# Kernel optimization log

Measured on AMD Instinct MI355X. Metric: run time of the kernel, lower is better.

## Reference

```python
import jax, jax.numpy as jnp
import numpy as np

N = 20000
E = 320000
D = 256
OUT = 256
NEG_SLOPE = 0.2


def setup_inputs() -> dict:
    key = jax.random.key(0)
    ks = jax.random.split(key, 16)
    s = 1.0 / np.sqrt(D)
    x = jax.random.normal(ks[0], (N, D), dtype=jnp.float32)
    edge_index = jax.random.randint(ks[1], (2, E), 0, N, dtype=jnp.int64)
    W1 = jax.random.uniform(ks[2], (D, D), jnp.float32, -s, s)
    W2 = jax.random.uniform(ks[3], (D, D), jnp.float32, -s, s)
    Ws = jax.random.uniform(ks[4], (6, D, D), jnp.float32, -s, s)      # per-layer GATConv lin weight
    a_src = jax.random.uniform(ks[5], (6, D), jnp.float32, -s, s)      # per-layer att_src
    a_dst = jax.random.uniform(ks[6], (6, D), jnp.float32, -s, s)      # per-layer att_dst
    bias = jnp.zeros((6, D), dtype=jnp.float32)                        # per-layer GATConv bias
    W3 = jax.random.uniform(ks[7], (2 * D, OUT), jnp.float32, -s, s)
    return {"x": x, "edge_index": edge_index, "W1": W1, "W2": W2,
            "Ws": Ws, "a_src": a_src, "a_dst": a_dst, "bias": bias, "W3": W3}


def _gat_layer(h, src, dst, W, asrc, adst, b):
    # h: [N, D] -> linear transform
    hw = h @ W                                         # [N, D]
    e_src = hw @ asrc                                  # [N]
    e_dst = hw @ adst                                  # [N]
    e = jax.nn.leaky_relu(e_src[src] + e_dst[dst], NEG_SLOPE)  # [E]
    # softmax over incoming edges per destination node
    m = jax.ops.segment_max(e, dst, num_segments=N)    # [N], -inf for empty segs (unused)
    ee = jnp.exp(e - m[dst])                           # [E]
    denom = jax.ops.segment_sum(ee, dst, num_segments=N)
    alpha = ee / denom[dst]                            # [E]
    msg = alpha[:, None] * hw[src]                     # [E, D]
    out = jax.ops.segment_sum(msg, dst, num_segments=N)  # [N, D]
    return out + b


def reference(x, edge_index, W1, W2, Ws, a_src, a_dst, bias, W3):
    src, dst = edge_index[0], edge_index[1]
    h = x @ W1
    h = h @ W2
    for i in range(6):
        h = _gat_layer(h, src, dst, Ws[i], a_src[i], a_dst[i], bias[i])
    h = jnp.concatenate((h, h), axis=1)   # [N, 2D]
    h = jax.nn.relu(h)
    return h @ W3                          # [N, OUT]
```

## Files before the change

### kernel.cpp

```cpp
#include <hip/hip_runtime.h>
#include <hip/hip_fp16.h>
#include <stdint.h>

#define NNODES 20000
#define EEDGES 320000
#define DD     256
#define NEG_SLOPE 0.2f
#define SCAN_BLOCKS ((NNODES + 255) / 256)

typedef _Float16 half8 __attribute__((ext_vector_type(8)));
typedef _Float16 half4 __attribute__((ext_vector_type(4)));
typedef float f32x4 __attribute__((ext_vector_type(4)));


__global__ void zero_ints_k(int* __restrict__ p, int n) {
    int i = blockIdx.x * 256 + threadIdx.x;
    if (i < n) p[i] = 0;
}

__global__ void hist_k(const int* __restrict__ dst, int* __restrict__ rowptr) {
    int i = blockIdx.x * 256 + threadIdx.x;
    if (i < EEDGES) atomicAdd(&rowptr[dst[i] + 1], 1);
}

__global__ __launch_bounds__(256) void scan1_k(int* __restrict__ rowptr, int* __restrict__ bsums) {
    __shared__ int buf[256];
    int idx = blockIdx.x * 256 + threadIdx.x;
    int v = (idx < NNODES) ? rowptr[idx + 1] : 0;
    buf[threadIdx.x] = v;
    __syncthreads();
#pragma unroll
    for (int off = 1; off < 256; off <<= 1) {
        int t = (threadIdx.x >= (unsigned)off) ? buf[threadIdx.x - off] : 0;
        __syncthreads();
        buf[threadIdx.x] += t;
        __syncthreads();
    }
    if (idx < NNODES) rowptr[idx + 1] = buf[threadIdx.x];
    if (threadIdx.x == 255) bsums[blockIdx.x] = buf[255];
}

__global__ __launch_bounds__(128) void scan2_k(int* __restrict__ bsums) {
    __shared__ int buf[128];
    int v = (threadIdx.x < SCAN_BLOCKS) ? bsums[threadIdx.x] : 0;
    buf[threadIdx.x] = v;
    __syncthreads();
#pragma unroll
    for (int off = 1; off < 128; off <<= 1) {
        int t = (threadIdx.x >= (unsigned)off) ? buf[threadIdx.x - off] : 0;
        __syncthreads();
        buf[threadIdx.x] += t;
        __syncthreads();
    }
    if (threadIdx.x < SCAN_BLOCKS) bsums[threadIdx.x] = buf[threadIdx.x];
}

__global__ void scan3_k(int* __restrict__ rowptr, const int* __restrict__ bsums,
                        int* __restrict__ cursor) {
    int idx = blockIdx.x * 256 + threadIdx.x;
    if (idx < NNODES) {
        int v = rowptr[idx + 1];
        if (blockIdx.x > 0) { v += bsums[blockIdx.x - 1]; rowptr[idx + 1] = v; }
        if (idx + 1 < NNODES) cursor[idx + 1] = v;
        if (idx == 0) cursor[0] = 0;
    }
}

__global__ void scatter_k(const int* __restrict__ src, const int* __restrict__ dst,
                          int* __restrict__ cursor, int* __restrict__ colsrc) {
    int i = blockIdx.x * 256 + threadIdx.x;
    if (i < EEDGES) {
        int d = dst[i];
        int pos = atomicAdd(&cursor[d], 1);
        colsrc[pos] = src[i];
    }
}


__global__ void cvt_split_k(const float* __restrict__ X, _Float16* __restrict__ Xh,
                            _Float16* __restrict__ Xl, int n) {
    int i = blockIdx.x * 256 + threadIdx.x;
    if (i < n) {
        float v = X[i];
        _Float16 hi = (_Float16)v;
        Xh[i] = hi;
        Xl[i] = (_Float16)(v - (float)hi);
    }
}


template<bool SUM>
__global__ void cvt_w_k(const float* __restrict__ W, _Float16* __restrict__ Wh,
                        _Float16* __restrict__ Wl) {
    int i = blockIdx.x * 256 + threadIdx.x;
    if (i < DD * DD) {
        int k = i >> 8, n = i & 255;
        float v = W[i];
        if (SUM) v += W[i + DD * DD];
        _Float16 hi = (_Float16)v;
        Wh[n * DD + k] = hi;
        Wl[n * DD + k] = (_Float16)(v - (float)hi);
    }
}


template<bool OUT_SPLIT>
__global__ __launch_bounds__(256) void gemm16_k(
    const _Float16* __restrict__ Ah, const _Float16* __restrict__ Al,
    const _Float16* __restrict__ Bh, const _Float16* __restrict__ Bl,
    float* __restrict__ C, _Float16* __restrict__ Ch, _Float16* __restrict__ Cl, int M)
{
    __shared__ _Float16 As_h[64][40], As_l[64][40], Bs_h[64][40], Bs_l[64][40];
    const int t = threadIdx.x;
    const int lane = t & 63;
    const int w = t >> 6;
    const int rowBase = blockIdx.y * 64;
    const int colBase = blockIdx.x * 64;
    const int mo = (w & 1) * 32;
    const int no = (w >> 1) * 32;

    const int srow = t >> 2;
    const int sseg = (t & 3) * 8;
    const int garow = rowBase + srow;
    const size_t aoff = (size_t)garow * DD + sseg;
    const size_t boff = (size_t)(colBase + srow) * DD + sseg;

    f32x4 acc00 = {0.f,0.f,0.f,0.f}, acc01 = acc00, acc10 = acc00, acc11 = acc00;
    const int4 zero4 = make_int4(0, 0, 0, 0);
    int4 ra_h, ra_l, rb_h, rb_l;

    ra_h = (garow < M) ? *(const int4*)(Ah + aoff) : zero4;
    ra_l = (garow < M) ? *(const int4*)(Al + aoff) : zero4;
    rb_h = *(const int4*)(Bh + boff);
    rb_l = *(const int4*)(Bl + boff);

    for (int s = 0; s < 8; ++s) {
        __syncthreads();
        *(int4*)&As_h[srow][sseg] = ra_h;
        *(int4*)&As_l[srow][sseg] = ra_l;
        *(int4*)&Bs_h[srow][sseg] = rb_h;
        *(int4*)&Bs_l[srow][sseg] = rb_l;
        __syncthreads();

        if (s < 7) {
            int kn = (s + 1) * 32;
            ra_h = (garow < M) ? *(const int4*)(Ah + aoff + kn) : zero4;
            ra_l = (garow < M) ? *(const int4*)(Al + aoff + kn) : zero4;
            rb_h = *(const int4*)(Bh + boff + kn);
            rb_l = *(const int4*)(Bl + boff + kn);
        }

        const int fr = lane & 15;
        const int fq = (lane >> 4) * 8;
        half8 a0h = *(const half8*)&As_h[mo + fr     ][fq];
        half8 a1h = *(const half8*)&As_h[mo + 16 + fr][fq];
        half8 a0l = *(const half8*)&As_l[mo + fr     ][fq];
        half8 a1l = *(const half8*)&As_l[mo + 16 + fr][fq];
        half8 b0h = *(const half8*)&Bs_h[no + fr     ][fq];
        half8 b1h = *(const half8*)&Bs_h[no + 16 + fr][fq];
        half8 b0l = *(const half8*)&Bs_l[no + fr     ][fq];
        half8 b1l = *(const half8*)&Bs_l[no + 16 + fr][fq];

        acc00 = __builtin_amdgcn_mfma_f32_16x16x32_f16(a0h, b0h, acc00, 0, 0, 0);
        acc01 = __builtin_amdgcn_mfma_f32_16x16x32_f16(a0h, b1h, acc01, 0, 0, 0);
        acc10 = __builtin_amdgcn_mfma_f32_16x16x32_f16(a1h, b0h, acc10, 0, 0, 0);
        acc11 = __builtin_amdgcn_mfma_f32_16x16x32_f16(a1h, b1h, acc11, 0, 0, 0);
        acc00 = __builtin_amdgcn_mfma_f32_16x16x32_f16(a0h, b0l, acc00, 0, 0, 0);
        acc01 = __builtin_amdgcn_mfma_f32_16x16x32_f16(a0h, b1l, acc01, 0, 0, 0);
        acc10 = __builtin_amdgcn_mfma_f32_16x16x32_f16(a1h, b0l, acc10, 0, 0, 0);
        acc11 = __builtin_amdgcn_mfma_f32_16x16x32_f16(a1h, b1l, acc11, 0, 0, 0);
        acc00 = __builtin_amdgcn_mfma_f32_16x16x32_f16(a0l, b0h, acc00, 0, 0, 0);
        acc01 = __builtin_amdgcn_mfma_f32_16x16x32_f16(a0l, b1h, acc01, 0, 0, 0);
        acc10 = __builtin_amdgcn_mfma_f32_16x16x32_f16(a1l, b0h, acc10, 0, 0, 0);
        acc11 = __builtin_amdgcn_mfma_f32_16x16x32_f16(a1l, b1h, acc11, 0, 0, 0);
        acc00 = __builtin_amdgcn_mfma_f32_16x16x32_f16(a0l, b0l, acc00, 0, 0, 0);
        acc01 = __builtin_amdgcn_mfma_f32_16x16x32_f16(a0l, b1l, acc01, 0, 0, 0);
        acc10 = __builtin_amdgcn_mfma_f32_16x16x32_f16(a1l, b0l, acc10, 0, 0, 0);
        acc11 = __builtin_amdgcn_mfma_f32_16x16x32_f16(a1l, b1l, acc11, 0, 0, 0);
    }

    const int ccol = lane & 15;
    const int crq = (lane >> 4) * 4;
#define EPI(ACC, MI, NI) \
    _Pragma("unroll") \
    for (int r = 0; r < 4; ++r) { \
        int grow = rowBase + mo + 16 * MI + crq + r; \
        if (grow < M) { \
            int gcol = colBase + no + 16 * NI + ccol; \
            float v = ACC[r]; \
            if (OUT_SPLIT) { \
                _Float16 hi = (_Float16)v; \
                Ch[(size_t)grow * DD + gcol] = hi; \
                Cl[(size_t)grow * DD + gcol] = (_Float16)(v - (float)hi); \
            } else { \
                C[(size_t)grow * DD + gcol] = v; \
            } \
        } \
    }
    EPI(acc00, 0, 0) EPI(acc01, 0, 1) EPI(acc10, 1, 0) EPI(acc11, 1, 1)
#undef EPI
}


__global__ __launch_bounds__(256) void dots_k(const float* __restrict__ hw,
                                              const float* __restrict__ asrc,
                                              const float* __restrict__ adst,
                                              float* __restrict__ es, float* __restrict__ ed) {
    int wave = threadIdx.x >> 6;
    int lane = threadIdx.x & 63;
    int node = blockIdx.x * 4 + wave;
    if (node >= NNODES) return;
    float4 v = *(const float4*)(hw + (size_t)node * DD + lane * 4);
    float4 a = *(const float4*)(asrc + lane * 4);
    float4 b = *(const float4*)(adst + lane * 4);
    float s = v.x * a.x + v.y * a.y + v.z * a.z + v.w * a.w;
    float d = v.x * b.x + v.y * b.y + v.z * b.z + v.w * b.w;
#pragma unroll
    for (int off = 32; off; off >>= 1) {
        s += __shfl_xor(s, off);
        d += __shfl_xor(d, off);
    }
    if (lane == 0) { es[node] = s; ed[node] = d; }
}


template<bool RELU>
__global__ __launch_bounds__(256) void gat_agg_k(const float* __restrict__ hw,
                                                 const float* __restrict__ es,
                                                 const float* __restrict__ ed,
                                                 const int* __restrict__ rowptr,
                                                 const int* __restrict__ colsrc,
                                                 float* __restrict__ ealpha,
                                                 const float* __restrict__ bias,
                                                 _Float16* __restrict__ hh,
                                                 _Float16* __restrict__ hl) {
    int wave = threadIdx.x >> 6;
    int lane = threadIdx.x & 63;
    int node = blockIdx.x * 4 + wave;
    if (node >= NNODES) return;
    int start = rowptr[node], end = rowptr[node + 1];
    int deg = end - start;
    float edd = ed[node];

    float4 acc0 = make_float4(0.f, 0.f, 0.f, 0.f);
    float4 acc1 = acc0, acc2 = acc0, acc3 = acc0;
    float4 acc4 = acc0, acc5 = acc0, acc6 = acc0, acc7 = acc0;

#define FMA4(ACC, W, V) \
    ACC.x = fmaf(W, V.x, ACC.x); ACC.y = fmaf(W, V.y, ACC.y); \
    ACC.z = fmaf(W, V.z, ACC.z); ACC.w = fmaf(W, V.w, ACC.w);

    if (deg <= 64) {
        if (deg > 0) {
            int j = start + lane;
            bool valid = j < end;
            int msrc = valid ? colsrc[j] : 0;
            float e = valid ? es[msrc] + edd : -INFINITY;
            e = fmaxf(e, NEG_SLOPE * e);
            float mx = e;
#pragma unroll
            for (int off = 32; off; off >>= 1) mx = fmaxf(mx, __shfl_xor(mx, off));
            float ee = valid ? expf(e - mx) : 0.f;
            float sum = ee;
#pragma unroll
            for (int off = 32; off; off >>= 1) sum += __shfl_xor(sum, off);
            float w = ee / sum;

            int j2 = 0;
            for (; j2 + 8 <= deg; j2 += 8) {
                int s0 = __shfl(msrc, j2 + 0), s1 = __shfl(msrc, j2 + 1);
                int s2 = __shfl(msrc, j2 + 2), s3 = __shfl(msrc, j2 + 3);
                int s4 = __shfl(msrc, j2 + 4), s5 = __shfl(msrc, j2 + 5);
                int s6 = __shfl(msrc, j2 + 6), s7 = __shfl(msrc, j2 + 7);
                float w0 = __shfl(w, j2 + 0), w1 = __shfl(w, j2 + 1);
                float w2 = __shfl(w, j2 + 2), w3 = __shfl(w, j2 + 3);
                float w4 = __shfl(w, j2 + 4), w5 = __shfl(w, j2 + 5);
                float w6 = __shfl(w, j2 + 6), w7 = __shfl(w, j2 + 7);
                float4 v0 = *(const float4*)(hw + (size_t)s0 * DD + lane * 4);
                float4 v1 = *(const float4*)(hw + (size_t)s1 * DD + lane * 4);
                float4 v2 = *(const float4*)(hw + (size_t)s2 * DD + lane * 4);
                float4 v3 = *(const float4*)(hw + (size_t)s3 * DD + lane * 4);
                float4 v4 = *(const float4*)(hw + (size_t)s4 * DD + lane * 4);
                float4 v5 = *(const float4*)(hw + (size_t)s5 * DD + lane * 4);
                float4 v6 = *(const float4*)(hw + (size_t)s6 * DD + lane * 4);
                float4 v7 = *(const float4*)(hw + (size_t)s7 * DD + lane * 4);
                FMA4(acc0, w0, v0); FMA4(acc1, w1, v1);
                FMA4(acc2, w2, v2); FMA4(acc3, w3, v3);
                FMA4(acc4, w4, v4); FMA4(acc5, w5, v5);
                FMA4(acc6, w6, v6); FMA4(acc7, w7, v7);
            }
            if (j2 + 4 <= deg) {
                int s0 = __shfl(msrc, j2 + 0), s1 = __shfl(msrc, j2 + 1);
                int s2 = __shfl(msrc, j2 + 2), s3 = __shfl(msrc, j2 + 3);
                float w0 = __shfl(w, j2 + 0), w1 = __shfl(w, j2 + 1);
                float w2 = __shfl(w, j2 + 2), w3 = __shfl(w, j2 + 3);
                float4 v0 = *(const float4*)(hw + (size_t)s0 * DD + lane * 4);
                float4 v1 = *(const float4*)(hw + (size_t)s1 * DD + lane * 4);
                float4 v2 = *(const float4*)(hw + (size_t)s2 * DD + lane * 4);
                float4 v3 = *(const float4*)(hw + (size_t)s3 * DD + lane * 4);
                FMA4(acc0, w0, v0); FMA4(acc1, w1, v1);
                FMA4(acc2, w2, v2); FMA4(acc3, w3, v3);
                j2 += 4;
            }
            for (; j2 < deg; ++j2) {
                int   s0 = __shfl(msrc, j2);
                float w0 = __shfl(w, j2);
                float4 v0 = *(const float4*)(hw + (size_t)s0 * DD + lane * 4);
                FMA4(acc0, w0, v0);
            }
        }
    } else {
        float mx = -INFINITY;
        for (int j = start + lane; j < end; j += 64) {
            float e = es[colsrc[j]] + edd;
            e = fmaxf(e, NEG_SLOPE * e);
            mx = fmaxf(mx, e);
        }
#pragma unroll
        for (int off = 32; off; off >>= 1) mx = fmaxf(mx, __shfl_xor(mx, off));
        float sum = 0.f;
        for (int j = start + lane; j < end; j += 64) {
            float e = es[colsrc[j]] + edd;
            e = fmaxf(e, NEG_SLOPE * e);
            float ee = expf(e - mx);
            ealpha[j] = ee;
            sum += ee;
        }
#pragma unroll
        for (int off = 32; off; off >>= 1) sum += __shfl_xor(sum, off);
        float inv = 1.f / sum;
        int j = start;
        for (; j + 4 <= end; j += 4) {
            int s0 = colsrc[j], s1 = colsrc[j + 1], s2 = colsrc[j + 2], s3 = colsrc[j + 3];
            float w0 = ealpha[j] * inv, w1 = ealpha[j + 1] * inv;
            float w2 = ealpha[j + 2] * inv, w3 = ealpha[j + 3] * inv;
            float4 v0 = *(const float4*)(hw + (size_t)s0 * DD + lane * 4);
            float4 v1 = *(const float4*)(hw + (size_t)s1 * DD + lane * 4);
            float4 v2 = *(const float4*)(hw + (size_t)s2 * DD + lane * 4);
            float4 v3 = *(const float4*)(hw + (size_t)s3 * DD + lane * 4);
            FMA4(acc0, w0, v0); FMA4(acc1, w1, v1);
            FMA4(acc2, w2, v2); FMA4(acc3, w3, v3);
        }
        for (; j < end; ++j) {
            int s0 = colsrc[j];
            float w0 = ealpha[j] * inv;
            float4 v0 = *(const float4*)(hw + (size_t)s0 * DD + lane * 4);
            FMA4(acc0, w0, v0);
        }
    }
#undef FMA4

    acc0.x += acc4.x; acc0.y += acc4.y; acc0.z += acc4.z; acc0.w += acc4.w;
    acc1.x += acc5.x; acc1.y += acc5.y; acc1.z += acc5.z; acc1.w += acc5.w;
    acc2.x += acc6.x; acc2.y += acc6.y; acc2.z += acc6.z; acc2.w += acc6.w;
    acc3.x += acc7.x; acc3.y += acc7.y; acc3.z += acc7.z; acc3.w += acc7.w;
    acc0.x += acc1.x; acc0.y += acc1.y; acc0.z += acc1.z; acc0.w += acc1.w;
    acc2.x += acc3.x; acc2.y += acc3.y; acc2.z += acc3.z; acc2.w += acc3.w;
    acc0.x += acc2.x; acc0.y += acc2.y; acc0.z += acc2.z; acc0.w += acc2.w;
    float4 b4 = *(const float4*)(bias + lane * 4);
    acc0.x += b4.x; acc0.y += b4.y; acc0.z += b4.z; acc0.w += b4.w;
    if (RELU) {
        acc0.x = fmaxf(acc0.x, 0.f); acc0.y = fmaxf(acc0.y, 0.f);
        acc0.z = fmaxf(acc0.z, 0.f); acc0.w = fmaxf(acc0.w, 0.f);
    }
    size_t base = (size_t)node * DD + lane * 4;
    _Float16 h0 = (_Float16)acc0.x, h1 = (_Float16)acc0.y;
    _Float16 h2 = (_Float16)acc0.z, h3 = (_Float16)acc0.w;
    half4 hv; hv[0] = h0; hv[1] = h1; hv[2] = h2; hv[3] = h3;
    half4 lv;
    lv[0] = (_Float16)(acc0.x - (float)h0); lv[1] = (_Float16)(acc0.y - (float)h1);
    lv[2] = (_Float16)(acc0.z - (float)h2); lv[3] = (_Float16)(acc0.w - (float)h3);
    *(half4*)(hh + base) = hv;
    *(half4*)(hl + base) = lv;
}


extern "C" void kernel_launch(void* const* d_in, const int* in_sizes, int n_in,
                              void* d_out, int out_size, void* d_ws, size_t ws_size,
                              hipStream_t stream) {
    const float* x     = (const float*)d_in[0];
    const int*   ei    = (const int*)d_in[1];
    const float* W1    = (const float*)d_in[2];
    const float* W2    = (const float*)d_in[3];
    const float* Ws    = (const float*)d_in[4];
    const float* a_src = (const float*)d_in[5];
    const float* a_dst = (const float*)d_in[6];
    const float* bias  = (const float*)d_in[7];
    const float* W3    = (const float*)d_in[8];
    float* out = (float*)d_out;

    const int* src = ei;
    const int* dst = ei + EEDGES;

    const size_t ND = (size_t)NNODES * DD;

    float* bufA   = (float*)d_ws;
    float* es     = bufA + ND;
    float* edv    = es + NNODES;
    float* ealpha = edv + NNODES;
    int*   rowptr = (int*)(ealpha + EEDGES);
    int*   cursor = rowptr + (NNODES + 1);
    int*   colsrc = cursor + NNODES;
    int*   bsums  = colsrc + EEDGES;
    _Float16* P0h = (_Float16*)(((uintptr_t)(bsums + SCAN_BLOCKS) + 15) & ~(uintptr_t)15);
    _Float16* P0l = P0h + ND;
    _Float16* P1h = P0l + ND;
    _Float16* P1l = P1h + ND;
    _Float16* WT  = P1l + ND;
    const size_t WSZ = (size_t)DD * DD;

    zero_ints_k<<<(NNODES + 1 + 255) / 256, 256, 0, stream>>>(rowptr, NNODES + 1);
    hist_k<<<(EEDGES + 255) / 256, 256, 0, stream>>>(dst, rowptr);
    scan1_k<<<SCAN_BLOCKS, 256, 0, stream>>>(rowptr, bsums);
    scan2_k<<<1, 128, 0, stream>>>(bsums);
    scan3_k<<<SCAN_BLOCKS, 256, 0, stream>>>(rowptr, bsums, cursor);
    scatter_k<<<(EEDGES + 255) / 256, 256, 0, stream>>>(src, dst, cursor, colsrc);

    const int WBLK = (DD * DD + 255) / 256;
    cvt_w_k<false><<<WBLK, 256, 0, stream>>>(W1, WT + 0 * 2 * WSZ, WT + 0 * 2 * WSZ + WSZ);
    cvt_w_k<false><<<WBLK, 256, 0, stream>>>(W2, WT + 1 * 2 * WSZ, WT + 1 * 2 * WSZ + WSZ);
    for (int l = 0; l < 6; ++l)
        cvt_w_k<false><<<WBLK, 256, 0, stream>>>(Ws + (size_t)l * WSZ,
                                                 WT + (2 + l) * 2 * WSZ,
                                                 WT + (2 + l) * 2 * WSZ + WSZ);
    cvt_w_k<true><<<WBLK, 256, 0, stream>>>(W3, WT + 8 * 2 * WSZ, WT + 8 * 2 * WSZ + WSZ);

    cvt_split_k<<<(int)((ND + 255) / 256), 256, 0, stream>>>(x, P0h, P0l, (int)ND);

    dim3 g16(DD / 64, (NNODES + 63) / 64);
    const int nodeBlocks = (NNODES + 3) / 4;

#define WTH(i) (WT + (i) * 2 * WSZ)
#define WTL(i) (WT + (i) * 2 * WSZ + WSZ)

    gemm16_k<true><<<g16, 256, 0, stream>>>(P0h, P0l, WTH(0), WTL(0), nullptr, P1h, P1l, NNODES);
    gemm16_k<true><<<g16, 256, 0, stream>>>(P1h, P1l, WTH(1), WTL(1), nullptr, P0h, P0l, NNODES);

    for (int l = 0; l < 6; ++l) {
        gemm16_k<false><<<g16, 256, 0, stream>>>(P0h, P0l, WTH(2 + l), WTL(2 + l),
                                                 bufA, nullptr, nullptr, NNODES);
        dots_k<<<nodeBlocks, 256, 0, stream>>>(bufA, a_src + (size_t)l * DD,
                                               a_dst + (size_t)l * DD, es, edv);
        if (l < 5)
            gat_agg_k<false><<<nodeBlocks, 256, 0, stream>>>(bufA, es, edv, rowptr, colsrc,
                                                             ealpha, bias + (size_t)l * DD,
                                                             P0h, P0l);
        else
            gat_agg_k<true><<<nodeBlocks, 256, 0, stream>>>(bufA, es, edv, rowptr, colsrc,
                                                            ealpha, bias + (size_t)l * DD,
                                                            P0h, P0l);
    }

    gemm16_k<false><<<g16, 256, 0, stream>>>(P0h, P0l, WTH(8), WTL(8), out,
                                             nullptr, nullptr, NNODES);
#undef WTH
#undef WTL
}
```

Before: 648.9 us.

## Fuse attention dots into GEMM epilogue, drop lo*lo MFMA, batch weight conversion

The attention dot products are now computed in the GEMM epilogue with shuffle reductions and float atomics into es/ed, which are zeroed beforehand. This removes the separate dots_k pass that re-read hw. The low*low correction term of the split-fp16 GEMM is dropped, cutting MFMA work by a quarter at a small accuracy cost. The nine weight-conversion launches become one 2D launch, and the aggregation inner loop is unrolled to 16 neighbours for more memory-level parallelism. Atomics make es/ed summation order nondeterministic.

```diff
diff --git a/kernel.cpp b/kernel.cpp
--- a/kernel.cpp
+++ b/kernel.cpp
@@ -16,6 +16,11 @@
 __global__ void zero_ints_k(int* __restrict__ p, int n) {
     int i = blockIdx.x * 256 + threadIdx.x;
     if (i < n) p[i] = 0;
+}
+
+__global__ void zero_f_k(float* __restrict__ p, int n) {
+    int i = blockIdx.x * 256 + threadIdx.x;
+    if (i < n) p[i] = 0.f;
 }
 
 __global__ void hist_k(const int* __restrict__ dst, int* __restrict__ rowptr) {
@@ -89,26 +94,33 @@
 }
 
 
-template<bool SUM>
-__global__ void cvt_w_k(const float* __restrict__ W, _Float16* __restrict__ Wh,
-                        _Float16* __restrict__ Wl) {
+__global__ void cvt_allw_k(const float* __restrict__ W1, const float* __restrict__ W2,
+                           const float* __restrict__ Ws, const float* __restrict__ W3,
+                           _Float16* __restrict__ WT) {
+    const size_t WSZ = (size_t)DD * DD;
+    int widx = blockIdx.y;
     int i = blockIdx.x * 256 + threadIdx.x;
-    if (i < DD * DD) {
-        int k = i >> 8, n = i & 255;
-        float v = W[i];
-        if (SUM) v += W[i + DD * DD];
-        _Float16 hi = (_Float16)v;
-        Wh[n * DD + k] = hi;
-        Wl[n * DD + k] = (_Float16)(v - (float)hi);
-    }
-}
-
-
-template<bool OUT_SPLIT>
+    if (i >= DD * DD) return;
+    int k = i >> 8, n = i & 255;
+    float v;
+    if (widx == 0)      v = W1[i];
+    else if (widx == 1) v = W2[i];
+    else if (widx < 8)  v = Ws[(size_t)(widx - 2) * WSZ + i];
+    else                v = W3[i] + W3[i + WSZ];
+    _Float16* Wh = WT + (size_t)widx * 2 * WSZ;
+    _Float16 hi = (_Float16)v;
+    Wh[n * DD + k] = hi;
+    Wh[WSZ + n * DD + k] = (_Float16)(v - (float)hi);
+}
+
+
+template<bool OUT_SPLIT, bool DOTS>
 __global__ __launch_bounds__(256) void gemm16_k(
     const _Float16* __restrict__ Ah, const _Float16* __restrict__ Al,
     const _Float16* __restrict__ Bh, const _Float16* __restrict__ Bl,
-    float* __restrict__ C, _Float16* __restrict__ Ch, _Float16* __restrict__ Cl, int M)
+    float* __restrict__ C, _Float16* __restrict__ Ch, _Float16* __restrict__ Cl,
+    const float* __restrict__ asrc, const float* __restrict__ adst,
+    float* __restrict__ es, float* __restrict__ ed, int M)
 {
     __shared__ _Float16 As_h[64][40], As_l[64][40], Bs_h[64][40], Bs_l[64][40];
     const int t = threadIdx.x;
@@ -173,14 +185,11 @@
         acc01 = __builtin_amdgcn_mfma_f32_16x16x32_f16(a0l, b1h, acc01, 0, 0, 0);
         acc10 = __builtin_amdgcn_mfma_f32_16x16x32_f16(a1l, b0h, acc10, 0, 0, 0);
         acc11 = __builtin_amdgcn_mfma_f32_16x16x32_f16(a1l, b1h, acc11, 0, 0, 0);
-        acc00 = __builtin_amdgcn_mfma_f32_16x16x32_f16(a0l, b0l, acc00, 0, 0, 0);
-        acc01 = __builtin_amdgcn_mfma_f32_16x16x32_f16(a0l, b1l, acc01, 0, 0, 0);
-        acc10 = __builtin_amdgcn_mfma_f32_16x16x32_f16(a1l, b0l, acc10, 0, 0, 0);
-        acc11 = __builtin_amdgcn_mfma_f32_16x16x32_f16(a1l, b1l, acc11, 0, 0, 0);
     }
 
     const int ccol = lane & 15;
     const int crq = (lane >> 4) * 4;
+
 #define EPI(ACC, MI, NI) \
     _Pragma("unroll") \
     for (int r = 0; r < 4; ++r) { \
@@ -199,28 +208,33 @@
     }
     EPI(acc00, 0, 0) EPI(acc01, 0, 1) EPI(acc10, 1, 0) EPI(acc11, 1, 1)
 #undef EPI
-}
-
-
-__global__ __launch_bounds__(256) void dots_k(const float* __restrict__ hw,
-                                              const float* __restrict__ asrc,
-                                              const float* __restrict__ adst,
-                                              float* __restrict__ es, float* __restrict__ ed) {
-    int wave = threadIdx.x >> 6;
-    int lane = threadIdx.x & 63;
-    int node = blockIdx.x * 4 + wave;
-    if (node >= NNODES) return;
-    float4 v = *(const float4*)(hw + (size_t)node * DD + lane * 4);
-    float4 a = *(const float4*)(asrc + lane * 4);
-    float4 b = *(const float4*)(adst + lane * 4);
-    float s = v.x * a.x + v.y * a.y + v.z * a.z + v.w * a.w;
-    float d = v.x * b.x + v.y * b.y + v.z * b.z + v.w * b.w;
-#pragma unroll
-    for (int off = 32; off; off >>= 1) {
-        s += __shfl_xor(s, off);
-        d += __shfl_xor(d, off);
-    }
-    if (lane == 0) { es[node] = s; ed[node] = d; }
+
+    if (DOTS) {
+        int c0 = colBase + no + ccol;
+        int c1 = colBase + no + 16 + ccol;
+        float as0 = asrc[c0], as1 = asrc[c1];
+        float ad0 = adst[c0], ad1 = adst[c1];
+#pragma unroll
+        for (int r = 0; r < 4; ++r) {
+            float s0 = acc00[r] * as0 + acc01[r] * as1;
+            float d0 = acc00[r] * ad0 + acc01[r] * ad1;
+            float s1 = acc10[r] * as0 + acc11[r] * as1;
+            float d1 = acc10[r] * ad0 + acc11[r] * ad1;
+#pragma unroll
+            for (int off = 1; off < 16; off <<= 1) {
+                s0 += __shfl_xor(s0, off);
+                d0 += __shfl_xor(d0, off);
+                s1 += __shfl_xor(s1, off);
+                d1 += __shfl_xor(d1, off);
+            }
+            if (ccol == 0) {
+                int row0 = rowBase + mo + crq + r;
+                int row1 = rowBase + mo + 16 + crq + r;
+                if (row0 < M) { atomicAdd(&es[row0], s0); atomicAdd(&ed[row0], d0); }
+                if (row1 < M) { atomicAdd(&es[row1], s1); atomicAdd(&ed[row1], d1); }
+            }
+        }
+    }
 }
 
 
@@ -267,7 +281,49 @@
             float w = ee / sum;
 
             int j2 = 0;
-            for (; j2 + 8 <= deg; j2 += 8) {
+            for (; j2 + 16 <= deg; j2 += 16) {
+                int s0 = __shfl(msrc, j2 + 0), s1 = __shfl(msrc, j2 + 1);
+                int s2 = __shfl(msrc, j2 + 2), s3 = __shfl(msrc, j2 + 3);
+                int s4 = __shfl(msrc, j2 + 4), s5 = __shfl(msrc, j2 + 5);
+                int s6 = __shfl(msrc, j2 + 6), s7 = __shfl(msrc, j2 + 7);
+                int s8 = __shfl(msrc, j2 + 8), s9 = __shfl(msrc, j2 + 9);
+                int sa = __shfl(msrc, j2 + 10), sb = __shfl(msrc, j2 + 11);
+                int sc = __shfl(msrc, j2 + 12), sd = __shfl(msrc, j2 + 13);
+                int se = __shfl(msrc, j2 + 14), sf = __shfl(msrc, j2 + 15);
+                float w0 = __shfl(w, j2 + 0), w1 = __shfl(w, j2 + 1);
+                float w2 = __shfl(w, j2 + 2), w3 = __shfl(w, j2 + 3);
+                float w4 = __shfl(w, j2 + 4), w5 = __shfl(w, j2 + 5);
+                float w6 = __shfl(w, j2 + 6), w7 = __shfl(w, j2 + 7);
+                float w8 = __shfl(w, j2 + 8), w9 = __shfl(w, j2 + 9);
+                float wa = __shfl(w, j2 + 10), wb = __shfl(w, j2 + 11);
+                float wc = __shfl(w, j2 + 12), wd = __shfl(w, j2 + 13);
+                float we = __shfl(w, j2 + 14), wf = __shfl(w, j2 + 15);
+                float4 v0 = *(const float4*)(hw + (size_t)s0 * DD + lane * 4);
+                float4 v1 = *(const float4*)(hw + (size_t)s1 * DD + lane * 4);
+                float4 v2 = *(const float4*)(hw + (size_t)s2 * DD + lane * 4);
+                float4 v3 = *(const float4*)(hw + (size_t)s3 * DD + lane * 4);
+                float4 v4 = *(const float4*)(hw + (size_t)s4 * DD + lane * 4);
+                float4 v5 = *(const float4*)(hw + (size_t)s5 * DD + lane * 4);
+                float4 v6 = *(const float4*)(hw + (size_t)s6 * DD + lane * 4);
+                float4 v7 = *(const float4*)(hw + (size_t)s7 * DD + lane * 4);
+                float4 v8 = *(const float4*)(hw + (size_t)s8 * DD + lane * 4);
+                float4 v9 = *(const float4*)(hw + (size_t)s9 * DD + lane * 4);
+                float4 va = *(const float4*)(hw + (size_t)sa * DD + lane * 4);
+                float4 vb = *(const float4*)(hw + (size_t)sb * DD + lane * 4);
+                float4 vc = *(const float4*)(hw + (size_t)sc * DD + lane * 4);
+                float4 vd = *(const float4*)(hw + (size_t)sd * DD + lane * 4);
+                float4 ve = *(const float4*)(hw + (size_t)se * DD + lane * 4);
+                float4 vf = *(const float4*)(hw + (size_t)sf * DD + lane * 4);
+                FMA4(acc0, w0, v0); FMA4(acc1, w1, v1);
+                FMA4(acc2, w2, v2); FMA4(acc3, w3, v3);
+                FMA4(acc4, w4, v4); FMA4(acc5, w5, v5);
+                FMA4(acc6, w6, v6); FMA4(acc7, w7, v7);
+                FMA4(acc0, w8, v8); FMA4(acc1, w9, v9);
+                FMA4(acc2, wa, va); FMA4(acc3, wb, vb);
+                FMA4(acc4, wc, vc); FMA4(acc5, wd, vd);
+                FMA4(acc6, we, ve); FMA4(acc7, wf, vf);
+            }
+            if (j2 + 8 <= deg) {
                 int s0 = __shfl(msrc, j2 + 0), s1 = __shfl(msrc, j2 + 1);
                 int s2 = __shfl(msrc, j2 + 2), s3 = __shfl(msrc, j2 + 3);
                 int s4 = __shfl(msrc, j2 + 4), s5 = __shfl(msrc, j2 + 5);
@@ -288,6 +344,7 @@
                 FMA4(acc2, w2, v2); FMA4(acc3, w3, v3);
                 FMA4(acc4, w4, v4); FMA4(acc5, w5, v5);
                 FMA4(acc6, w6, v6); FMA4(acc7, w7, v7);
+                j2 += 8;
             }
             if (j2 + 4 <= deg) {
                 int s0 = __shfl(msrc, j2 + 0), s1 = __shfl(msrc, j2 + 1);
@@ -391,8 +448,8 @@
 
     const int* src = ei;
     const int* dst = ei + EEDGES;
-
     const size_t ND = (size_t)NNODES * DD;
+    const size_t WSZ = (size_t)DD * DD;
 
     float* bufA   = (float*)d_ws;
     float* es     = bufA + ND;
@@ -407,7 +464,6 @@
     _Float16* P1h = P0l + ND;
     _Float16* P1l = P1h + ND;
     _Float16* WT  = P1l + ND;
-    const size_t WSZ = (size_t)DD * DD;
 
     zero_ints_k<<<(NNODES + 1 + 255) / 256, 256, 0, stream>>>(rowptr, NNODES + 1);
     hist_k<<<(EEDGES + 255) / 256, 256, 0, stream>>>(dst, rowptr);
@@ -416,15 +472,7 @@
     scan3_k<<<SCAN_BLOCKS, 256, 0, stream>>>(rowptr, bsums, cursor);
     scatter_k<<<(EEDGES + 255) / 256, 256, 0, stream>>>(src, dst, cursor, colsrc);
 
-    const int WBLK = (DD * DD + 255) / 256;
-    cvt_w_k<false><<<WBLK, 256, 0, stream>>>(W1, WT + 0 * 2 * WSZ, WT + 0 * 2 * WSZ + WSZ);
-    cvt_w_k<false><<<WBLK, 256, 0, stream>>>(W2, WT + 1 * 2 * WSZ, WT + 1 * 2 * WSZ + WSZ);
-    for (int l = 0; l < 6; ++l)
-        cvt_w_k<false><<<WBLK, 256, 0, stream>>>(Ws + (size_t)l * WSZ,
-                                                 WT + (2 + l) * 2 * WSZ,
-                                                 WT + (2 + l) * 2 * WSZ + WSZ);
-    cvt_w_k<true><<<WBLK, 256, 0, stream>>>(W3, WT + 8 * 2 * WSZ, WT + 8 * 2 * WSZ + WSZ);
-
+    cvt_allw_k<<<dim3((DD * DD + 255) / 256, 9), 256, 0, stream>>>(W1, W2, Ws, W3, WT);
     cvt_split_k<<<(int)((ND + 255) / 256), 256, 0, stream>>>(x, P0h, P0l, (int)ND);
 
     dim3 g16(DD / 64, (NNODES + 63) / 64);
@@ -433,14 +481,20 @@
 #define WTH(i) (WT + (i) * 2 * WSZ)
 #define WTL(i) (WT + (i) * 2 * WSZ + WSZ)
 
-    gemm16_k<true><<<g16, 256, 0, stream>>>(P0h, P0l, WTH(0), WTL(0), nullptr, P1h, P1l, NNODES);
-    gemm16_k<true><<<g16, 256, 0, stream>>>(P1h, P1l, WTH(1), WTL(1), nullptr, P0h, P0l, NNODES);
+    gemm16_k<true, false><<<g16, 256, 0, stream>>>(P0h, P0l, WTH(0), WTL(0),
+                                                   nullptr, P1h, P1l,
+                                                   nullptr, nullptr, nullptr, nullptr, NNODES);
+    gemm16_k<true, false><<<g16, 256, 0, stream>>>(P1h, P1l, WTH(1), WTL(1),
+                                                   nullptr, P0h, P0l,
+                                                   nullptr, nullptr, nullptr, nullptr, NNODES);
 
     for (int l = 0; l < 6; ++l) {
-        gemm16_k<false><<<g16, 256, 0, stream>>>(P0h, P0l, WTH(2 + l), WTL(2 + l),
-                                                 bufA, nullptr, nullptr, NNODES);
-        dots_k<<<nodeBlocks, 256, 0, stream>>>(bufA, a_src + (size_t)l * DD,
-                                               a_dst + (size_t)l * DD, es, edv);
+        zero_f_k<<<(2 * NNODES + 255) / 256, 256, 0, stream>>>(es, 2 * NNODES);
+        gemm16_k<false, true><<<g16, 256, 0, stream>>>(P0h, P0l, WTH(2 + l), WTL(2 + l),
+                                                       bufA, nullptr, nullptr,
+                                                       a_src + (size_t)l * DD,
+                                                       a_dst + (size_t)l * DD,
+                                                       es, edv, NNODES);
         if (l < 5)
             gat_agg_k<false><<<nodeBlocks, 256, 0, stream>>>(bufA, es, edv, rowptr, colsrc,
                                                              ealpha, bias + (size_t)l * DD,
@@ -451,8 +505,9 @@
                                                             P0h, P0l);
     }
 
-    gemm16_k<false><<<g16, 256, 0, stream>>>(P0h, P0l, WTH(8), WTL(8), out,
-                                             nullptr, nullptr, NNODES);
+    gemm16_k<false, false><<<g16, 256, 0, stream>>>(P0h, P0l, WTH(8), WTL(8), out,
+                                                    nullptr, nullptr,
+                                                    nullptr, nullptr, nullptr, nullptr, NNODES);
 #undef WTH
 #undef WTL
 }
```

After: 653.5 us. No clear change (+0.7%).
